# Kernel tuning notes

Measured on AMD Instinct MI355X. Metric: run time of the kernel, lower is better.

## Reference

```python
import jax, jax.numpy as jnp
import numpy as np

HEADS = 4
DIM_HEAD = 64
QUERY_DIM = 512
CONTEXT_DIM = 512
INNER = HEADS * DIM_HEAD  # 256
SCALE = DIM_HEAD ** -0.5


def setup_inputs() -> dict:
    key = jax.random.key(0)
    ks = jax.random.split(key, 9)
    b, n, m = 4, 2048, 2048
    inp = {
        'x1': jax.random.normal(ks[0], (b, n, QUERY_DIM), jnp.float32),
        'x2': jax.random.normal(ks[1], (b, n, QUERY_DIM), jnp.float32),
        'context': jax.random.normal(ks[2], (b, m, CONTEXT_DIM), jnp.float32),
        # weights stored [in, out] (= torch weight.T)
        'Wq': jax.random.normal(ks[3], (QUERY_DIM, INNER), jnp.float32) * (QUERY_DIM ** -0.5),
        'Wq2': jax.random.normal(ks[4], (QUERY_DIM, INNER), jnp.float32) * (QUERY_DIM ** -0.5),
        'Wk': jax.random.normal(ks[5], (CONTEXT_DIM, INNER), jnp.float32) * (CONTEXT_DIM ** -0.5),
        'Wv': jax.random.normal(ks[6], (CONTEXT_DIM, INNER), jnp.float32) * (CONTEXT_DIM ** -0.5),
        'Wo': jax.random.normal(ks[7], (INNER, QUERY_DIM), jnp.float32) * (INNER ** -0.5),
        'bo': jax.random.normal(ks[8], (QUERY_DIM,), jnp.float32) * 0.01,
    }
    return inp


def _split_heads(t):
    # [b, n, h*d] -> [b, h, n, d]
    b, n, _ = t.shape
    return t.reshape(b, n, HEADS, DIM_HEAD).transpose(0, 2, 1, 3)


def reference(x1, x2, context, Wq, Wq2, Wk, Wv, Wo, bo):
    q = _split_heads(x1 @ Wq)
    q2 = _split_heads(x2 @ Wq2)
    k = _split_heads(context @ Wk)
    v = _split_heads(context @ Wv)
    sim = jnp.einsum('bhid,bhjd->bhij', q, k) * SCALE
    sim2 = jnp.einsum('bhid,bhjd->bhij', q2, k) * SCALE
    attn = 0.3 * jax.nn.softmax(sim, axis=-1) + 0.7 * jax.nn.softmax(sim2, axis=-1)
    out = jnp.einsum('bhij,bhjd->bhid', attn, v)  # [b, h, n, d]
    b, h, n, d = out.shape
    out = out.transpose(0, 2, 1, 3).reshape(b, n, h * d)
    return out @ Wo + bo
```

## Files before the change

### kernel.cpp

```cpp
#include <hip/hip_runtime.h>

typedef __attribute__((ext_vector_type(8))) short bf16x8;
typedef __attribute__((ext_vector_type(4))) float f32x4;
typedef unsigned short ushort_t;
typedef unsigned int uint_t;

__device__ __forceinline__ ushort_t f2bf(float f) {
    unsigned int x = __builtin_bit_cast(unsigned int, f);
    x += 0x7fffu + ((x >> 16) & 1u);
    return (ushort_t)(x >> 16);
}
__device__ __forceinline__ uint_t pack2(float a, float b) {
    return (uint_t)f2bf(a) | ((uint_t)f2bf(b) << 16);
}

#define LOG2E 1.4426950408889634f

#define WT_OFF   0
#define WOT_OFF  524288
#define QKV_OFF  655360
#define QKV_SZ   2097152
#define QKV_OFF_Z3 (3 * (size_t)QKV_SZ)
#define O_OFF    9043968

__global__ __launch_bounds__(256) void transpose_w(
    const float* __restrict__ Wq, const float* __restrict__ Wq2,
    const float* __restrict__ Wk, const float* __restrict__ Wv,
    const float* __restrict__ Wo, ushort_t* __restrict__ ws)
{
    const int j = blockIdx.y;
    const int t = blockIdx.x * 256 + threadIdx.x;
    const float* in;
    ushort_t* out;
    int C;
    if (j < 4) {
        in = (j == 0) ? Wq : (j == 1) ? Wq2 : (j == 2) ? Wk : Wv;
        out = ws + WT_OFF + (size_t)j * 131072;
        C = 256;
    } else {
        in = Wo; out = ws + WOT_OFF; C = 512;
    }
    const int R = 131072 / C;
    const int r = t / C, c = t % C;
    out[(size_t)c * R + r] = f2bf(in[t]);
}

__global__ __launch_bounds__(256) void proj_gemm(
    const float* __restrict__ x1, const float* __restrict__ x2,
    const float* __restrict__ ctx, const ushort_t* __restrict__ Wt,
    ushort_t* __restrict__ QKV)
{
    __shared__ __align__(16) ushort_t lA[64 * 40];
    __shared__ __align__(16) ushort_t lB[256 * 40];
    const int z = blockIdx.y;
    const float* A = (z == 0) ? x1 : (z == 1) ? x2 : ctx;
    const ushort_t* Bt = Wt + (size_t)z * 131072;
    const float sc = (z < 2) ? (0.125f * LOG2E) : 1.0f;
    const int tid = threadIdx.x;
    const int wave = tid >> 6, lane = tid & 63;
    const int quad = lane >> 4, l16 = lane & 15;
    const size_t row0 = (size_t)blockIdx.x * 64;
    const int sr = tid >> 2, sc8 = (tid & 3) << 3;

    f32x4 acc[16] = {};
    for (int k0 = 0; k0 < 512; k0 += 32) {
        const float* src = A + (row0 + sr) * 512 + k0 + sc8;
        float4 v0 = *(const float4*)src;
        float4 v1 = *(const float4*)(src + 4);
        ushort_t tmp[8] = { f2bf(v0.x), f2bf(v0.y), f2bf(v0.z), f2bf(v0.w),
                            f2bf(v1.x), f2bf(v1.y), f2bf(v1.z), f2bf(v1.w) };
        *(uint4*)&lA[sr * 40 + sc8] = *(const uint4*)tmp;
#pragma unroll
        for (int rr = 0; rr < 4; ++rr)
            *(uint4*)&lB[(rr * 64 + sr) * 40 + sc8] =
                *(const uint4*)(Bt + (size_t)(rr * 64 + sr) * 512 + k0 + sc8);
        __syncthreads();
        bf16x8 af = *(const bf16x8*)&lA[(wave * 16 + l16) * 40 + quad * 8];
#pragma unroll
        for (int c = 0; c < 16; ++c) {
            bf16x8 bfr = *(const bf16x8*)&lB[(c * 16 + l16) * 40 + quad * 8];
            acc[c] = __builtin_amdgcn_mfma_f32_16x16x32_bf16(af, bfr, acc[c], 0, 0, 0);
        }
        __syncthreads();
    }
    if (z == 3) {
        const int b = (int)(row0 >> 11);
        const int tokl = ((int)row0 & 2047) + wave * 16 + quad * 4;
        ushort_t* Vt = QKV + QKV_OFF_Z3;
#pragma unroll
        for (int c = 0; c < 16; ++c) {
            const int col = c * 16 + l16;
            const int h = col >> 6, d = col & 63;
            uint2 w;
            w.x = pack2(acc[c][0], acc[c][1]);
            w.y = pack2(acc[c][2], acc[c][3]);
            *(uint2*)(Vt + ((size_t)((b * 4 + h) * 64 + d)) * 2048 + tokl) = w;
        }
    } else {
        ushort_t* C = QKV + (size_t)z * QKV_SZ;
#pragma unroll
        for (int c = 0; c < 16; ++c) {
            const int col = c * 16 + l16;
#pragma unroll
            for (int r = 0; r < 4; ++r)
                C[(row0 + wave * 16 + quad * 4 + r) * 256 + col] = f2bf(acc[c][r] * sc);
        }
    }
}

__global__ __launch_bounds__(256) void out_gemm(
    const ushort_t* __restrict__ Op, const ushort_t* __restrict__ Wot,
    const float* __restrict__ bias, float* __restrict__ out)
{
    __shared__ __align__(16) ushort_t lA[64 * 40];
    __shared__ __align__(16) ushort_t lB[256 * 40];
    const int tid = threadIdx.x;
    const int wave = tid >> 6, lane = tid & 63;
    const int quad = lane >> 4, l16 = lane & 15;
    const size_t row0 = (size_t)blockIdx.x * 64;
    const int col0 = blockIdx.y * 256;
    const int sr = tid >> 2, sc8 = (tid & 3) << 3;

    f32x4 acc[16] = {};
    for (int k0 = 0; k0 < 256; k0 += 32) {
        *(uint4*)&lA[sr * 40 + sc8] = *(const uint4*)(Op + (row0 + sr) * 256 + k0 + sc8);
#pragma unroll
        for (int rr = 0; rr < 4; ++rr)
            *(uint4*)&lB[(rr * 64 + sr) * 40 + sc8] =
                *(const uint4*)(Wot + (size_t)(col0 + rr * 64 + sr) * 256 + k0 + sc8);
        __syncthreads();
        bf16x8 af = *(const bf16x8*)&lA[(wave * 16 + l16) * 40 + quad * 8];
#pragma unroll
        for (int c = 0; c < 16; ++c) {
            bf16x8 bfr = *(const bf16x8*)&lB[(c * 16 + l16) * 40 + quad * 8];
            acc[c] = __builtin_amdgcn_mfma_f32_16x16x32_bf16(af, bfr, acc[c], 0, 0, 0);
        }
        __syncthreads();
    }
#pragma unroll
    for (int c = 0; c < 16; ++c) {
        const int col = col0 + c * 16 + l16;
        const float bv = bias[col];
#pragma unroll
        for (int r = 0; r < 4; ++r)
            out[(row0 + wave * 16 + quad * 4 + r) * 512 + col] = acc[c][r] + bv;
    }
}


#define ATTN_STAGE(MB, BUF) do {                                                        \
    _Pragma("unroll")                                                                   \
    for (int it_ = 0; it_ < 2; ++it_) {                                                 \
        const int cc_ = tid + it_ * 256;                                                \
        const int g_ = (cc_ ^ (cc_ >> 3)) & 7;                                          \
        const ushort_t* kp_ = Kb + (size_t)(tok0 + (MB) + (cc_ >> 3)) * 256 + in0 + g_ * 8; \
        __builtin_amdgcn_global_load_lds(                                               \
            (const __attribute__((address_space(1))) void*)kp_,                         \
            (__attribute__((address_space(3))) void*)&lK[BUF][cc_ * 8], 16, 0, 0);      \
        const ushort_t* vp_ = Vt + (size_t)(bh64 + (cc_ >> 3)) * 2048 + (MB) + g_ * 8;  \
        __builtin_amdgcn_global_load_lds(                                               \
            (const __attribute__((address_space(1))) void*)vp_,                         \
            (__attribute__((address_space(3))) void*)&lV[BUF][cc_ * 8], 16, 0, 0);      \
    }                                                                                   \
} while (0)

#define ATTN_ITER(I, P) do {                                                            \
    __syncthreads();                                                                    \
    { const int mn_ = ((I) + 1) * 64; if (mn_ < 2048) ATTN_STAGE(mn_, 1 - (P)); }       \
    f32x4 st1[4] = {}, st2[4] = {};                                                     \
    _Pragma("unroll")                                                                   \
    for (int c = 0; c < 4; ++c) {                                                       \
        _Pragma("unroll")                                                               \
        for (int ks = 0; ks < 2; ++ks) {                                                \
            bf16x8 kf = *(const bf16x8*)&lK[P][(c * 16 + l16) * 64 +                    \
                                              ((((ks * 4 + quad) ^ l7) & 7) << 3)];     \
            st1[c] = __builtin_amdgcn_mfma_f32_16x16x32_bf16(kf, q1f[ks], st1[c], 0, 0, 0); \
            st2[c] = __builtin_amdgcn_mfma_f32_16x16x32_bf16(kf, q2f[ks], st2[c], 0, 0, 0); \
        } }                                                                             \
    _Pragma("unroll")                                                                   \
    for (int c = 0; c < 4; ++c) {                                                       \
        float p0 = __builtin_amdgcn_exp2f(st1[c][0]);                                   \
        float p1 = __builtin_amdgcn_exp2f(st1[c][1]);                                   \
        float p2 = __builtin_amdgcn_exp2f(st1[c][2]);                                   \
        float p3 = __builtin_amdgcn_exp2f(st1[c][3]);                                   \
        l1 += (p0 + p1) + (p2 + p3);                                                    \
        uint2 w; w.x = pack2(p0, p1); w.y = pack2(p2, p3);                              \
        *(uint2*)&lPw0[l16 * 72 + c * 16 + quad * 4] = w;                               \
        float r0 = __builtin_amdgcn_exp2f(st2[c][0]);                                   \
        float r1 = __builtin_amdgcn_exp2f(st2[c][1]);                                   \
        float r2 = __builtin_amdgcn_exp2f(st2[c][2]);                                   \
        float r3 = __builtin_amdgcn_exp2f(st2[c][3]);                                   \
        l2 += (r0 + r1) + (r2 + r3);                                                    \
        uint2 y; y.x = pack2(r0, r1); y.y = pack2(r2, r3);                              \
        *(uint2*)&lPw1[l16 * 72 + c * 16 + quad * 4] = y;                               \
    }                                                                                   \
    bf16x8 pa1[2], pa2[2];                                                              \
    _Pragma("unroll")                                                                   \
    for (int ks = 0; ks < 2; ++ks) {                                                    \
        pa1[ks] = *(const bf16x8*)&lPw0[l16 * 72 + ks * 32 + quad * 8];                 \
        pa2[ks] = *(const bf16x8*)&lPw1[l16 * 72 + ks * 32 + quad * 8];                 \
    }                                                                                   \
    _Pragma("unroll")                                                                   \
    for (int c = 0; c < 4; ++c) {                                                       \
        _Pragma("unroll")                                                               \
        for (int ks = 0; ks < 2; ++ks) {                                                \
            bf16x8 vf = *(const bf16x8*)&lV[P][(c * 16 + l16) * 64 +                    \
                                              ((((ks * 4 + quad) ^ l7) & 7) << 3)];     \
            o1[c] = __builtin_amdgcn_mfma_f32_16x16x32_bf16(vf, pa1[ks], o1[c], 0, 0, 0); \
            o2[c] = __builtin_amdgcn_mfma_f32_16x16x32_bf16(vf, pa2[ks], o2[c], 0, 0, 0); \
        } }                                                                             \
} while (0)

__global__ __launch_bounds__(256) void attn_fused(
    const ushort_t* __restrict__ Qb, const ushort_t* __restrict__ Q2b,
    const ushort_t* __restrict__ Kb, const ushort_t* __restrict__ Vt,
    ushort_t* __restrict__ Ob)
{
    __shared__ __align__(16) ushort_t lK[2][64 * 64];
    __shared__ __align__(16) ushort_t lV[2][64 * 64];
    __shared__ __align__(16) ushort_t lP[4][2][16 * 72];

    const int qt = blockIdx.x;
    const int bh = blockIdx.y;
    const int tid = threadIdx.x;
    const int wave = tid >> 6, lane = tid & 63;
    const int quad = lane >> 4, l16 = lane & 15;
    const int l7 = l16 & 7;
    const size_t tok0 = (size_t)(bh >> 2) * 2048;
    const int in0 = (bh & 3) * 64;
    const int bh64 = bh * 64;
    ushort_t* lPw0 = &lP[wave][0][0];
    ushort_t* lPw1 = &lP[wave][1][0];

    bf16x8 q1f[2], q2f[2];
    {
        const ushort_t* qr1 = Qb  + (tok0 + qt * 64 + wave * 16 + l16) * 256 + in0;
        const ushort_t* qr2 = Q2b + (tok0 + qt * 64 + wave * 16 + l16) * 256 + in0;
#pragma unroll
        for (int ks = 0; ks < 2; ++ks) {
            q1f[ks] = *(const bf16x8*)(qr1 + ks * 32 + quad * 8);
            q2f[ks] = *(const bf16x8*)(qr2 + ks * 32 + quad * 8);
        }
    }

    ATTN_STAGE(0, 0);

    f32x4 o1[4] = {}, o2[4] = {};
    float l1 = 0.f, l2 = 0.f;

    for (int i = 0; i < 32; i += 2) {
        ATTN_ITER(i, 0);
        ATTN_ITER(i + 1, 1);
    }

    l1 += __shfl_xor(l1, 16, 64); l1 += __shfl_xor(l1, 32, 64);
    l2 += __shfl_xor(l2, 16, 64); l2 += __shfl_xor(l2, 32, 64);
    const float inv1 = 0.3f / l1, inv2 = 0.7f / l2;

    ushort_t* orow = Ob + (tok0 + qt * 64 + wave * 16 + l16) * 256 + in0;
#pragma unroll
    for (int c = 0; c < 4; ++c) {
        const float f0 = o1[c][0] * inv1 + o2[c][0] * inv2;
        const float f1 = o1[c][1] * inv1 + o2[c][1] * inv2;
        const float f2 = o1[c][2] * inv1 + o2[c][2] * inv2;
        const float f3 = o1[c][3] * inv1 + o2[c][3] * inv2;
        uint2 w; w.x = pack2(f0, f1); w.y = pack2(f2, f3);
        *(uint2*)(orow + c * 16 + quad * 4) = w;
    }
}

extern "C" void kernel_launch(void* const* d_in, const int* in_sizes, int n_in,
                              void* d_out, int out_size, void* d_ws, size_t ws_size,
                              hipStream_t stream)
{
    (void)in_sizes; (void)n_in; (void)out_size; (void)ws_size;
    const float* x1  = (const float*)d_in[0];
    const float* x2  = (const float*)d_in[1];
    const float* ctx = (const float*)d_in[2];
    const float* Wq  = (const float*)d_in[3];
    const float* Wq2 = (const float*)d_in[4];
    const float* Wk  = (const float*)d_in[5];
    const float* Wv  = (const float*)d_in[6];
    const float* Wo  = (const float*)d_in[7];
    const float* bo  = (const float*)d_in[8];
    ushort_t* ws  = (ushort_t*)d_ws;
    float* out = (float*)d_out;

    ushort_t* Wt  = ws + WT_OFF;
    ushort_t* Wot = ws + WOT_OFF;
    ushort_t* QKV = ws + QKV_OFF;
    ushort_t* Q   = QKV;
    ushort_t* Q2  = QKV + 1 * (size_t)QKV_SZ;
    ushort_t* Kp  = QKV + 2 * (size_t)QKV_SZ;
    ushort_t* Vt  = QKV + 3 * (size_t)QKV_SZ;
    ushort_t* Op  = ws + O_OFF;

    transpose_w<<<dim3(512, 5), 256, 0, stream>>>(Wq, Wq2, Wk, Wv, Wo, ws);
    proj_gemm  <<<dim3(128, 4), 256, 0, stream>>>(x1, x2, ctx, Wt, QKV);
    attn_fused <<<dim3(32, 16), 256, 0, stream>>>(Q, Q2, Kp, Vt, Op);
    out_gemm   <<<dim3(128, 2), 256, 0, stream>>>(Op, Wot, bo, out);
}
```

Baseline: 195.6 us.

## Double-buffer GEMM B tiles via direct LDS loads and tile weight transpose

```diff
diff --git a/kernel.cpp b/kernel.cpp
--- a/kernel.cpp
+++ b/kernel.cpp
@@ -6,9 +6,7 @@
 typedef unsigned int uint_t;
 
 __device__ __forceinline__ ushort_t f2bf(float f) {
-    unsigned int x = __builtin_bit_cast(unsigned int, f);
-    x += 0x7fffu + ((x >> 16) & 1u);
-    return (ushort_t)(x >> 16);
+    return __builtin_bit_cast(ushort_t, (__bf16)f);
 }
 __device__ __forceinline__ uint_t pack2(float a, float b) {
     return (uint_t)f2bf(a) | ((uint_t)f2bf(b) << 16);
@@ -28,30 +26,57 @@
     const float* __restrict__ Wk, const float* __restrict__ Wv,
     const float* __restrict__ Wo, ushort_t* __restrict__ ws)
 {
+    __shared__ ushort_t lT[64][72];
     const int j = blockIdx.y;
-    const int t = blockIdx.x * 256 + threadIdx.x;
+    const int bx = blockIdx.x;
     const float* in;
     ushort_t* out;
     int C;
     if (j < 4) {
         in = (j == 0) ? Wq : (j == 1) ? Wq2 : (j == 2) ? Wk : Wv;
-        out = ws + WT_OFF + (size_t)j * 131072;
-        C = 256;
+        out = ws + WT_OFF + (size_t)j * 131072; C = 256;
     } else {
         in = Wo; out = ws + WOT_OFF; C = 512;
     }
     const int R = 131072 / C;
-    const int r = t / C, c = t % C;
-    out[(size_t)c * R + r] = f2bf(in[t]);
-}
+    const int tc = C >> 6;
+    const int r0 = (bx / tc) * 64, c0 = (bx % tc) * 64;
+    const int t = threadIdx.x;
+    const int ir = t >> 4, ic = (t & 15) * 4;
+#pragma unroll
+    for (int i = 0; i < 4; ++i) {
+        const int r = ir + i * 16;
+        float4 v = *(const float4*)(in + (size_t)(r0 + r) * C + c0 + ic);
+        uint2 w; w.x = pack2(v.x, v.y); w.y = pack2(v.z, v.w);
+        *(uint2*)&lT[r][ic] = w;
+    }
+    __syncthreads();
+    const int oc = t >> 2, rr0 = (t & 3) * 16;
+    ushort_t g[16];
+#pragma unroll
+    for (int k = 0; k < 16; ++k) g[k] = lT[rr0 + k][oc];
+    ushort_t* op = out + (size_t)(c0 + oc) * R + r0 + rr0;
+    *(uint4*)op = *(const uint4*)&g[0];
+    *(uint4*)(op + 8) = *(const uint4*)&g[8];
+}
+
+#define PROJ_STAGE(K0, BUF) do {                                                     \
+    _Pragma("unroll")                                                                \
+    for (int it_ = 0; it_ < 4; ++it_) {                                              \
+        const int p_ = tid + it_ * 256;                                              \
+        const ushort_t* bp_ = Bt + (size_t)(p_ >> 2) * 512 + (K0) + ((p_ & 3) << 3); \
+        __builtin_amdgcn_global_load_lds(                                            \
+            (const __attribute__((address_space(1))) void*)bp_,                      \
+            (__attribute__((address_space(3))) void*)&lB[BUF][p_ * 8], 16, 0, 0);    \
+    }                                                                                \
+} while (0)
 
 __global__ __launch_bounds__(256) void proj_gemm(
     const float* __restrict__ x1, const float* __restrict__ x2,
     const float* __restrict__ ctx, const ushort_t* __restrict__ Wt,
     ushort_t* __restrict__ QKV)
 {
-    __shared__ __align__(16) ushort_t lA[64 * 40];
-    __shared__ __align__(16) ushort_t lB[256 * 40];
+    __shared__ __align__(16) ushort_t lB[2][256 * 32];
     const int z = blockIdx.y;
     const float* A = (z == 0) ? x1 : (z == 1) ? x2 : ctx;
     const ushort_t* Bt = Wt + (size_t)z * 131072;
@@ -60,29 +85,35 @@
     const int wave = tid >> 6, lane = tid & 63;
     const int quad = lane >> 4, l16 = lane & 15;
     const size_t row0 = (size_t)blockIdx.x * 64;
-    const int sr = tid >> 2, sc8 = (tid & 3) << 3;
+
+    PROJ_STAGE(0, 0);
+
+    const float* arow = A + (row0 + wave * 16 + l16) * 512 + quad * 8;
+    float4 a0 = *(const float4*)(arow);
+    float4 a1 = *(const float4*)(arow + 4);
 
     f32x4 acc[16] = {};
     for (int k0 = 0; k0 < 512; k0 += 32) {
-        const float* src = A + (row0 + sr) * 512 + k0 + sc8;
-        float4 v0 = *(const float4*)src;
-        float4 v1 = *(const float4*)(src + 4);
-        ushort_t tmp[8] = { f2bf(v0.x), f2bf(v0.y), f2bf(v0.z), f2bf(v0.w),
-                            f2bf(v1.x), f2bf(v1.y), f2bf(v1.z), f2bf(v1.w) };
-        *(uint4*)&lA[sr * 40 + sc8] = *(const uint4*)tmp;
-#pragma unroll
-        for (int rr = 0; rr < 4; ++rr)
-            *(uint4*)&lB[(rr * 64 + sr) * 40 + sc8] =
-                *(const uint4*)(Bt + (size_t)(rr * 64 + sr) * 512 + k0 + sc8);
+        const int pb = (k0 >> 5) & 1;
         __syncthreads();
-        bf16x8 af = *(const bf16x8*)&lA[(wave * 16 + l16) * 40 + quad * 8];
+        if (k0 + 32 < 512) PROJ_STAGE(k0 + 32, 1 - pb);
+        float4 n0 = a0, n1 = a1;
+        if (k0 + 32 < 512) {
+            n0 = *(const float4*)(arow + k0 + 32);
+            n1 = *(const float4*)(arow + k0 + 36);
+        }
+        uint4 aw;
+        aw.x = pack2(a0.x, a0.y); aw.y = pack2(a0.z, a0.w);
+        aw.z = pack2(a1.x, a1.y); aw.w = pack2(a1.z, a1.w);
+        bf16x8 af = __builtin_bit_cast(bf16x8, aw);
 #pragma unroll
         for (int c = 0; c < 16; ++c) {
-            bf16x8 bfr = *(const bf16x8*)&lB[(c * 16 + l16) * 40 + quad * 8];
+            bf16x8 bfr = *(const bf16x8*)&lB[pb][(c * 16 + l16) * 32 + quad * 8];
             acc[c] = __builtin_amdgcn_mfma_f32_16x16x32_bf16(af, bfr, acc[c], 0, 0, 0);
         }
-        __syncthreads();
-    }
+        a0 = n0; a1 = n1;
+    }
+
     if (z == 3) {
         const int b = (int)(row0 >> 11);
         const int tokl = ((int)row0 & 2047) + wave * 16 + quad * 4;
@@ -108,37 +139,48 @@
     }
 }
 
+#define OUT_STAGE(K0, BUF) do {                                                      \
+    _Pragma("unroll")                                                                \
+    for (int it_ = 0; it_ < 2; ++it_) {                                              \
+        const int p_ = tid + it_ * 256;                                              \
+        const ushort_t* bp_ = Wot + (size_t)(col0 + (p_ >> 2)) * 256 + (K0) + ((p_ & 3) << 3); \
+        __builtin_amdgcn_global_load_lds(                                            \
+            (const __attribute__((address_space(1))) void*)bp_,                      \
+            (__attribute__((address_space(3))) void*)&lB[BUF][p_ * 8], 16, 0, 0);    \
+    }                                                                                \
+} while (0)
+
 __global__ __launch_bounds__(256) void out_gemm(
     const ushort_t* __restrict__ Op, const ushort_t* __restrict__ Wot,
     const float* __restrict__ bias, float* __restrict__ out)
 {
-    __shared__ __align__(16) ushort_t lA[64 * 40];
-    __shared__ __align__(16) ushort_t lB[256 * 40];
+    __shared__ __align__(16) ushort_t lB[2][128 * 32];
     const int tid = threadIdx.x;
     const int wave = tid >> 6, lane = tid & 63;
     const int quad = lane >> 4, l16 = lane & 15;
     const size_t row0 = (size_t)blockIdx.x * 64;
-    const int col0 = blockIdx.y * 256;
-    const int sr = tid >> 2, sc8 = (tid & 3) << 3;
-
-    f32x4 acc[16] = {};
+    const int col0 = blockIdx.y * 128;
+
+    OUT_STAGE(0, 0);
+    const ushort_t* arow = Op + (row0 + wave * 16 + l16) * 256 + quad * 8;
+    bf16x8 af = *(const bf16x8*)(arow);
+
+    f32x4 acc[8] = {};
     for (int k0 = 0; k0 < 256; k0 += 32) {
-        *(uint4*)&lA[sr * 40 + sc8] = *(const uint4*)(Op + (row0 + sr) * 256 + k0 + sc8);
-#pragma unroll
-        for (int rr = 0; rr < 4; ++rr)
-            *(uint4*)&lB[(rr * 64 + sr) * 40 + sc8] =
-                *(const uint4*)(Wot + (size_t)(col0 + rr * 64 + sr) * 256 + k0 + sc8);
+        const int pb = (k0 >> 5) & 1;
         __syncthreads();
-        bf16x8 af = *(const bf16x8*)&lA[(wave * 16 + l16) * 40 + quad * 8];
-#pragma unroll
-        for (int c = 0; c < 16; ++c) {
-            bf16x8 bfr = *(const bf16x8*)&lB[(c * 16 + l16) * 40 + quad * 8];
+        if (k0 + 32 < 256) OUT_STAGE(k0 + 32, 1 - pb);
+        bf16x8 an = af;
+        if (k0 + 32 < 256) an = *(const bf16x8*)(arow + k0 + 32);
+#pragma unroll
+        for (int c = 0; c < 8; ++c) {
+            bf16x8 bfr = *(const bf16x8*)&lB[pb][(c * 16 + l16) * 32 + quad * 8];
             acc[c] = __builtin_amdgcn_mfma_f32_16x16x32_bf16(af, bfr, acc[c], 0, 0, 0);
         }
-        __syncthreads();
-    }
-#pragma unroll
-    for (int c = 0; c < 16; ++c) {
+        af = an;
+    }
+#pragma unroll
+    for (int c = 0; c < 8; ++c) {
         const int col = col0 + c * 16 + l16;
         const float bv = bias[col];
 #pragma unroll
@@ -295,8 +337,8 @@
     ushort_t* Vt  = QKV + 3 * (size_t)QKV_SZ;
     ushort_t* Op  = ws + O_OFF;
 
-    transpose_w<<<dim3(512, 5), 256, 0, stream>>>(Wq, Wq2, Wk, Wv, Wo, ws);
+    transpose_w<<<dim3(32, 5),  256, 0, stream>>>(Wq, Wq2, Wk, Wv, Wo, ws);
     proj_gemm  <<<dim3(128, 4), 256, 0, stream>>>(x1, x2, ctx, Wt, QKV);
     attn_fused <<<dim3(32, 16), 256, 0, stream>>>(Q, Q2, Kp, Vt, Op);
-    out_gemm   <<<dim3(128, 2), 256, 0, stream>>>(Op, Wot, bo, out);
-}
+    out_gemm   <<<dim3(128, 4), 256, 0, stream>>>(Op, Wot, bo, out);
+}
```

After: 182.2 us. -6.9%, faster.
